# Performance work log

Measured on AMD Instinct MI355X. Metric: run time of the kernel, lower is better.

The kernel has to match this reference:

```python
import jax, jax.numpy as jnp
import numpy as np

N = 4096
D = 128
NUM_INSTANCES = 8  # samples per class in the balanced batch


def setup_inputs() -> dict:
    key = jax.random.key(0)
    x = jax.random.normal(key, (N, D), dtype=jnp.float32)
    # L2-normalize embeddings (keeps sim in [-1,1] so exp(40*sim) is finite)
    inputs = x / jnp.linalg.norm(x, axis=1, keepdims=True)
    # balanced batch: NUM_INSTANCES consecutive samples per class
    targets = (jnp.arange(N) // NUM_INSTANCES).astype(jnp.int64)
    return {"inputs": inputs, "targets": targets, "num_instances": NUM_INSTANCES}


def reference(inputs, targets, num_instances):
    n = inputs.shape[0]
    k = num_instances - 1          # positives per row (excluding self)
    sim = inputs @ inputs.T        # [n, n]

    eye = jnp.eye(n, dtype=bool)
    pos_mask = (targets[:, None] == targets[None, :]) & ~eye
    # category per entry: 0 = positive, 1 = negative, 2 = diagonal
    cat = jnp.where(pos_mask, 0, jnp.where(eye, 2, 1))
    order = jnp.argsort(cat, axis=1, stable=True)  # row-major masked_select order
    sorted_sim = jnp.take_along_axis(sim, order, axis=1)

    pos = jnp.sort(sorted_sim[:, :k], axis=1)          # [n, k]
    neg = jnpp_sort = jnp.sort(sorted_sim[:, k:n - 1], axis=1)  # [n, n-1-k]

    # GaussDistribution used .data[0] -> detached scalars (no grad through stats)
    pos_mean = jax.lax.stop_gradient(jnp.mean(pos, axis=1))
    pos_std = jax.lax.stop_gradient(jnp.sqrt(jnp.mean((pos - pos_mean[:, None]) ** 2, axis=1)))
    neg_mean = jax.lax.stop_gradient(jnp.mean(neg, axis=1))
    neg_std = jax.lax.stop_gradient(jnp.sqrt(jnp.mean((neg - neg_mean[:, None]) ** 2, axis=1)))

    inter = (neg_std * pos_mean + pos_std * neg_mean) / (pos_std + neg_std)
    inter = 0.8 * inter + 0.1                           # [n]

    pos_loss = 0.2 * jnp.mean(jnp.log1p(jnp.exp(-10.0 * (pos - inter[:, None]))), axis=1)

    # keep only negatives above (min positive - 0.05); masked mean per row
    keep = neg > (pos[:, :1] - 0.05)                    # [n, n-1-k] bool
    neg_vals = jnp.log1p(jnp.exp(40.0 * (neg - inter[:, None])))
    cnt = jnp.sum(keep, axis=1)
    neg_loss = 0.05 * jnp.sum(jnp.where(keep, neg_vals, 0.0), axis=1) / jnp.maximum(cnt, 1)

    return jnp.sum(pos_loss + neg_loss) / n
```

## Files before the change

kernel.cpp:

```cpp
#include <hip/hip_runtime.h>
#include <math.h>

namespace {

constexpr int N     = 4096;
constexpr int D     = 128;
constexpr int M     = 8;
constexpr int ROWS  = 16;
constexpr int NT    = 1024;
constexpr int NWAVE = NT / 64;
constexpr int TR    = 256;
constexpr int TBYTES = TR * D * 2;
constexpr int NTILE = N / TR;

using short8 = __attribute__((ext_vector_type(8))) short;
using f32x4  = __attribute__((ext_vector_type(4))) float;

__device__ __forceinline__ float bf2f(unsigned short u) {
    unsigned v = (unsigned)u << 16;
    return __builtin_bit_cast(float, v);
}
__device__ __forceinline__ unsigned short f2bf(float f) {
    unsigned u = __builtin_bit_cast(unsigned, f);
    u += 0x7FFFu + ((u >> 16) & 1u);
    return (unsigned short)(u >> 16);
}
__device__ __forceinline__ float sp_fast(float z) {
    return fmaxf(z, 0.f) + __logf(1.f + __expf(-fabsf(z)));
}

__device__ __forceinline__ void gl_lds16(const void* g, void* l) {
    __builtin_amdgcn_global_load_lds(
        (const __attribute__((address_space(1))) unsigned int*)g,
        (__attribute__((address_space(3))) unsigned int*)l,
        16, 0, 0);
}

__global__ void cvt_kernel(const float* __restrict__ X,
                           unsigned short* __restrict__ Xb,
                           float* __restrict__ out)
{
    const int i = blockIdx.x * blockDim.x + threadIdx.x;
    if (i == 0) out[0] = 0.f;
    const float4 v = reinterpret_cast<const float4*>(X)[i];
    ushort4 r;
    r.x = f2bf(v.x); r.y = f2bf(v.y); r.z = f2bf(v.z); r.w = f2bf(v.w);
    reinterpret_cast<ushort4*>(Xb)[i] = r;
}

__global__ __launch_bounds__(NT, 4)
void mdl_kernel(const unsigned short* __restrict__ Xb, float* __restrict__ out)
{
    extern __shared__ char smem[];
    unsigned short* Bt = reinterpret_cast<unsigned short*>(smem);
    float* posLds = reinterpret_cast<float*>(smem + 2 * TBYTES);
    float* red    = posLds + ROWS * M;
    float* stat   = red + NWAVE * ROWS * 2;

    const int t    = threadIdx.x;
    const int lane = t & 63;
    const int w    = t >> 6;
    const int lr   = lane & 15;
    const int lg   = lane >> 4;
    const int bid  = blockIdx.x;
    const int R0   = bid * ROWS;

    const char* XbB = reinterpret_cast<const char*>(Xb);

    short8 afr0, afr1, afr2, afr3;
    {
        const unsigned short* qrow = Xb + (size_t)(R0 + lr) * D + lg * 8;
        afr0 = *reinterpret_cast<const short8*>(qrow);
        afr1 = *reinterpret_cast<const short8*>(qrow + 32);
        afr2 = *reinterpret_cast<const short8*>(qrow + 64);
        afr3 = *reinterpret_cast<const short8*>(qrow + 96);
    }

    auto STAGE = [&](int tile, int buf) {
        const char* src = XbB + (size_t)tile * TBYTES;
        char* dstb = reinterpret_cast<char*>(Bt) + buf * TBYTES + w * 4096;
#pragma unroll
        for (int r = 0; r < 4; ++r) {
            const int o  = w * 4096 + r * 1024 + lane * 16;
            const int so = o ^ (((o >> 8) & 7) << 4);
            gl_lds16(src + so, dstb + r * 1024);
        }
    };

    float sum4[4] = {0.f, 0.f, 0.f, 0.f};
    float sq4[4]  = {0.f, 0.f, 0.f, 0.f};
    unsigned pk0[NTILE], pk1[NTILE];

    STAGE(0, 0);
    __syncthreads();

#pragma unroll
    for (int k = 0; k < NTILE; ++k) {
        if (k + 1 < NTILE) STAGE(k + 1, (k + 1) & 1);

        const char* bufb  = reinterpret_cast<const char*>(Bt) + (k & 1) * TBYTES;
        const int rowoff  = (w * 16 + lr) * 256;
        const int csw     = (lr & 7) << 4;
        short8 b0 = *reinterpret_cast<const short8*>(bufb + rowoff + ((  0 + lg * 16) ^ csw));
        short8 b1 = *reinterpret_cast<const short8*>(bufb + rowoff + (( 64 + lg * 16) ^ csw));
        short8 b2 = *reinterpret_cast<const short8*>(bufb + rowoff + ((128 + lg * 16) ^ csw));
        short8 b3 = *reinterpret_cast<const short8*>(bufb + rowoff + ((192 + lg * 16) ^ csw));

        f32x4 acc = {0.f, 0.f, 0.f, 0.f};
        acc = __builtin_amdgcn_mfma_f32_16x16x32_bf16(afr0, b0, acc, 0, 0, 0);
        acc = __builtin_amdgcn_mfma_f32_16x16x32_bf16(afr1, b1, acc, 0, 0, 0);
        acc = __builtin_amdgcn_mfma_f32_16x16x32_bf16(afr2, b2, acc, 0, 0, 0);
        acc = __builtin_amdgcn_mfma_f32_16x16x32_bf16(afr3, b3, acc, 0, 0, 0);

        const int chunk = k * 16 + w;
        const bool cls  = (chunk == bid) && ((lr >> 3) == (lg >> 1));
        if (!cls) {
#pragma unroll
            for (int i = 0; i < 4; ++i) {
                const float v = acc[i];
                sum4[i] += v; sq4[i] += v * v;
            }
        } else {
#pragma unroll
            for (int i = 0; i < 4; ++i)
                posLds[(lg * 4 + i) * M + (lr & 7)] = acc[i];
        }
        pk0[k] = (unsigned)f2bf(acc[0]) | ((unsigned)f2bf(acc[1]) << 16);
        pk1[k] = (unsigned)f2bf(acc[2]) | ((unsigned)f2bf(acc[3]) << 16);

        __syncthreads();
    }

#pragma unroll
    for (int i = 0; i < 4; ++i) {
        float s = sum4[i], q = sq4[i];
#pragma unroll
        for (int off = 8; off; off >>= 1) {
            s += __shfl_down(s, off, 16);
            q += __shfl_down(q, off, 16);
        }
        if (lr == 0) {
            red[(w * ROWS + lg * 4 + i) * 2]     = s;
            red[(w * ROWS + lg * 4 + i) * 2 + 1] = q;
        }
    }
    __syncthreads();

    if (t < ROWS) {
        const int r = t;
        float tot = 0.f, totsq = 0.f;
        for (int ww = 0; ww < NWAVE; ++ww) {
            tot   += red[(ww * ROWS + r) * 2];
            totsq += red[(ww * ROWS + r) * 2 + 1];
        }
        float psum = 0.f, psq = 0.f, pmin = 1e30f;
        for (int p = 0; p < M; ++p) {
            if (p == (r & 7)) continue;
            const float s = posLds[r * M + p];
            psum += s; psq += s * s; pmin = fminf(pmin, s);
        }
        const float kinv  = 1.f / (float)(M - 1);
        const float pmean = psum * kinv;
        const float pstd  = sqrtf(fmaxf(psq * kinv - pmean * pmean, 0.f));
        const float ninv  = 1.f / (float)(N - M);
        const float nmean = tot * ninv;
        const float nstd  = sqrtf(fmaxf(totsq * ninv - nmean * nmean, 0.f));
        float inter = (nstd * pmean + pstd * nmean) / (pstd + nstd);
        inter = 0.8f * inter + 0.1f;

        float pl = 0.f;
        for (int p = 0; p < M; ++p) {
            if (p == (r & 7)) continue;
            pl += sp_fast(-10.f * (posLds[r * M + p] - inter));
        }
        pl *= 0.2f * kinv;

        stat[r * 4 + 0] = inter;
        stat[r * 4 + 1] = pmin - 0.05f;
        stat[r * 4 + 2] = pl;
    }
    __syncthreads();

    float itr4[4], thr4[4];
#pragma unroll
    for (int i = 0; i < 4; ++i) {
        itr4[i] = stat[(lg * 4 + i) * 4 + 0];
        thr4[i] = stat[(lg * 4 + i) * 4 + 1];
    }
    float nls[4] = {0.f, 0.f, 0.f, 0.f};
    float cnt[4] = {0.f, 0.f, 0.f, 0.f};

#pragma unroll
    for (int k = 0; k < NTILE; ++k) {
        const int chunk = k * 16 + w;
        const bool cls  = (chunk == bid) && ((lr >> 3) == (lg >> 1));
#pragma unroll
        for (int i = 0; i < 4; ++i) {
            const unsigned pkw = (i < 2) ? pk0[k] : pk1[k];
            const float v = bf2f((unsigned short)(pkw >> ((i & 1) * 16)));
            if (!cls && v > thr4[i]) {
                cnt[i] += 1.f;
                nls[i] += sp_fast(40.f * (v - itr4[i]));
            }
        }
    }

#pragma unroll
    for (int i = 0; i < 4; ++i) {
        float s = nls[i], c = cnt[i];
#pragma unroll
        for (int off = 8; off; off >>= 1) {
            s += __shfl_down(s, off, 16);
            c += __shfl_down(c, off, 16);
        }
        if (lr == 0) {
            red[(w * ROWS + lg * 4 + i) * 2]     = s;
            red[(w * ROWS + lg * 4 + i) * 2 + 1] = c;
        }
    }
    __syncthreads();

    if (t < ROWS) {
        float a = 0.f, b = 0.f;
        for (int ww = 0; ww < NWAVE; ++ww) {
            a += red[(ww * ROWS + t) * 2];
            b += red[(ww * ROWS + t) * 2 + 1];
        }
        stat[t * 4 + 3] = stat[t * 4 + 2] + 0.05f * a / fmaxf(b, 1.f);
    }
    __syncthreads();

    if (t == 0) {
        float acc = 0.f;
        for (int r = 0; r < ROWS; ++r) acc += stat[r * 4 + 3];
        atomicAdd(out, acc * (1.f / (float)N));
    }
}

}

extern "C" void kernel_launch(void* const* d_in, const int* in_sizes, int n_in,
                              void* d_out, int out_size, void* d_ws, size_t ws_size,
                              hipStream_t stream)
{
    const float* X = (const float*)d_in[0];
    float* out = (float*)d_out;
    unsigned short* Xb = (unsigned short*)d_ws;

    cvt_kernel<<<dim3(N * D / 4 / 256), dim3(256), 0, stream>>>(X, Xb, out);

    const size_t shmem = (size_t)2 * TBYTES
                       + (size_t)(ROWS * M) * 4
                       + (size_t)(NWAVE * ROWS * 2) * 4
                       + (size_t)(ROWS * 4) * 4;
    (void)hipFuncSetAttribute(reinterpret_cast<const void*>(mdl_kernel),
                              hipFuncAttributeMaxDynamicSharedMemorySize, (int)shmem);

    mdl_kernel<<<dim3(N / ROWS), dim3(NT), shmem, stream>>>(Xb, out);
}
```

Measured before the change: 93.48 us.

## Load B fragments directly from global with register double-buffering, drop LDS staging

Replaces the LDS-staged, swizzled tile pipeline (global_load_lds plus a barrier per tile) with direct per-wave global loads of B fragments into registers, double-buffered across 16 chunks. This removes the 16 block-wide barriers and the large dynamic LDS allocation, which may allow more resident blocks. It also switches bf16 packing to the HIP intrinsic. The cost is more register pressure and reliance on L2/L1 for reuse of the 1 MB bf16 matrix that all 256 blocks read, with uncoalesced 16-byte row loads.

```diff
diff --git a/kernel.cpp b/kernel.cpp
--- a/kernel.cpp
+++ b/kernel.cpp
@@ -1,4 +1,5 @@
 #include <hip/hip_runtime.h>
+#include <hip/hip_bf16.h>
 #include <math.h>
 
 namespace {
@@ -9,9 +10,7 @@
 constexpr int ROWS  = 16;
 constexpr int NT    = 1024;
 constexpr int NWAVE = NT / 64;
-constexpr int TR    = 256;
-constexpr int TBYTES = TR * D * 2;
-constexpr int NTILE = N / TR;
+constexpr int NCH   = 16;
 
 using short8 = __attribute__((ext_vector_type(8))) short;
 using f32x4  = __attribute__((ext_vector_type(4))) float;
@@ -28,12 +27,11 @@
 __device__ __forceinline__ float sp_fast(float z) {
     return fmaxf(z, 0.f) + __logf(1.f + __expf(-fabsf(z)));
 }
-
-__device__ __forceinline__ void gl_lds16(const void* g, void* l) {
-    __builtin_amdgcn_global_load_lds(
-        (const __attribute__((address_space(1))) unsigned int*)g,
-        (__attribute__((address_space(3))) unsigned int*)l,
-        16, 0, 0);
+__device__ __forceinline__ unsigned pack_bf(float lo, float hi) {
+    __hip_bfloat162 h = __float22bfloat162_rn(make_float2(lo, hi));
+    unsigned u;
+    __builtin_memcpy(&u, &h, 4);
+    return u;
 }
 
 __global__ void cvt_kernel(const float* __restrict__ X,
@@ -51,11 +49,9 @@
 __global__ __launch_bounds__(NT, 4)
 void mdl_kernel(const unsigned short* __restrict__ Xb, float* __restrict__ out)
 {
-    extern __shared__ char smem[];
-    unsigned short* Bt = reinterpret_cast<unsigned short*>(smem);
-    float* posLds = reinterpret_cast<float*>(smem + 2 * TBYTES);
-    float* red    = posLds + ROWS * M;
-    float* stat   = red + NWAVE * ROWS * 2;
+    __shared__ float posLds[ROWS * M];
+    __shared__ float red[NWAVE * ROWS * 2];
+    __shared__ float stat[ROWS * 4];
 
     const int t    = threadIdx.x;
     const int lane = t & 63;
@@ -65,8 +61,6 @@
     const int bid  = blockIdx.x;
     const int R0   = bid * ROWS;
 
-    const char* XbB = reinterpret_cast<const char*>(Xb);
-
     short8 afr0, afr1, afr2, afr3;
     {
         const unsigned short* qrow = Xb + (size_t)(R0 + lr) * D + lg * 8;
@@ -76,43 +70,34 @@
         afr3 = *reinterpret_cast<const short8*>(qrow + 96);
     }
 
-    auto STAGE = [&](int tile, int buf) {
-        const char* src = XbB + (size_t)tile * TBYTES;
-        char* dstb = reinterpret_cast<char*>(Bt) + buf * TBYTES + w * 4096;
-#pragma unroll
-        for (int r = 0; r < 4; ++r) {
-            const int o  = w * 4096 + r * 1024 + lane * 16;
-            const int so = o ^ (((o >> 8) & 7) << 4);
-            gl_lds16(src + so, dstb + r * 1024);
-        }
-    };
+    const unsigned short* bbase = Xb + (size_t)(w * 16 + lr) * D + lg * 8;
 
     float sum4[4] = {0.f, 0.f, 0.f, 0.f};
     float sq4[4]  = {0.f, 0.f, 0.f, 0.f};
-    unsigned pk0[NTILE], pk1[NTILE];
-
-    STAGE(0, 0);
-    __syncthreads();
-
-#pragma unroll
-    for (int k = 0; k < NTILE; ++k) {
-        if (k + 1 < NTILE) STAGE(k + 1, (k + 1) & 1);
-
-        const char* bufb  = reinterpret_cast<const char*>(Bt) + (k & 1) * TBYTES;
-        const int rowoff  = (w * 16 + lr) * 256;
-        const int csw     = (lr & 7) << 4;
-        short8 b0 = *reinterpret_cast<const short8*>(bufb + rowoff + ((  0 + lg * 16) ^ csw));
-        short8 b1 = *reinterpret_cast<const short8*>(bufb + rowoff + (( 64 + lg * 16) ^ csw));
-        short8 b2 = *reinterpret_cast<const short8*>(bufb + rowoff + ((128 + lg * 16) ^ csw));
-        short8 b3 = *reinterpret_cast<const short8*>(bufb + rowoff + ((192 + lg * 16) ^ csw));
+    unsigned pk0[NCH], pk1[NCH];
+
+    short8 bf[2][4];
+#pragma unroll
+    for (int kk = 0; kk < 4; ++kk)
+        bf[0][kk] = *reinterpret_cast<const short8*>(bbase + kk * 32);
+
+#pragma unroll
+    for (int cc = 0; cc < NCH; ++cc) {
+        const int cur = cc & 1, nxt = cur ^ 1;
+        if (cc + 1 < NCH) {
+            const unsigned short* nb = bbase + (size_t)(cc + 1) * 256 * D;
+#pragma unroll
+            for (int kk = 0; kk < 4; ++kk)
+                bf[nxt][kk] = *reinterpret_cast<const short8*>(nb + kk * 32);
+        }
 
         f32x4 acc = {0.f, 0.f, 0.f, 0.f};
-        acc = __builtin_amdgcn_mfma_f32_16x16x32_bf16(afr0, b0, acc, 0, 0, 0);
-        acc = __builtin_amdgcn_mfma_f32_16x16x32_bf16(afr1, b1, acc, 0, 0, 0);
-        acc = __builtin_amdgcn_mfma_f32_16x16x32_bf16(afr2, b2, acc, 0, 0, 0);
-        acc = __builtin_amdgcn_mfma_f32_16x16x32_bf16(afr3, b3, acc, 0, 0, 0);
-
-        const int chunk = k * 16 + w;
+        acc = __builtin_amdgcn_mfma_f32_16x16x32_bf16(afr0, bf[cur][0], acc, 0, 0, 0);
+        acc = __builtin_amdgcn_mfma_f32_16x16x32_bf16(afr1, bf[cur][1], acc, 0, 0, 0);
+        acc = __builtin_amdgcn_mfma_f32_16x16x32_bf16(afr2, bf[cur][2], acc, 0, 0, 0);
+        acc = __builtin_amdgcn_mfma_f32_16x16x32_bf16(afr3, bf[cur][3], acc, 0, 0, 0);
+
+        const int chunk = cc * 16 + w;
         const bool cls  = (chunk == bid) && ((lr >> 3) == (lg >> 1));
         if (!cls) {
 #pragma unroll
@@ -125,10 +110,8 @@
             for (int i = 0; i < 4; ++i)
                 posLds[(lg * 4 + i) * M + (lr & 7)] = acc[i];
         }
-        pk0[k] = (unsigned)f2bf(acc[0]) | ((unsigned)f2bf(acc[1]) << 16);
-        pk1[k] = (unsigned)f2bf(acc[2]) | ((unsigned)f2bf(acc[3]) << 16);
-
-        __syncthreads();
+        pk0[cc] = pack_bf(acc[0], acc[1]);
+        pk1[cc] = pack_bf(acc[2], acc[3]);
     }
 
 #pragma unroll
@@ -191,12 +174,12 @@
     float cnt[4] = {0.f, 0.f, 0.f, 0.f};
 
 #pragma unroll
-    for (int k = 0; k < NTILE; ++k) {
-        const int chunk = k * 16 + w;
+    for (int cc = 0; cc < NCH; ++cc) {
+        const int chunk = cc * 16 + w;
         const bool cls  = (chunk == bid) && ((lr >> 3) == (lg >> 1));
 #pragma unroll
         for (int i = 0; i < 4; ++i) {
-            const unsigned pkw = (i < 2) ? pk0[k] : pk1[k];
+            const unsigned pkw = (i < 2) ? pk0[cc] : pk1[cc];
             const float v = bf2f((unsigned short)(pkw >> ((i & 1) * 16)));
             if (!cls && v > thr4[i]) {
                 cnt[i] += 1.f;
@@ -248,13 +231,5 @@
     unsigned short* Xb = (unsigned short*)d_ws;
 
     cvt_kernel<<<dim3(N * D / 4 / 256), dim3(256), 0, stream>>>(X, Xb, out);
-
-    const size_t shmem = (size_t)2 * TBYTES
-                       + (size_t)(ROWS * M) * 4
-                       + (size_t)(NWAVE * ROWS * 2) * 4
-                       + (size_t)(ROWS * 4) * 4;
-    (void)hipFuncSetAttribute(reinterpret_cast<const void*>(mdl_kernel),
-                              hipFuncAttributeMaxDynamicSharedMemorySize, (int)shmem);
-
-    mdl_kernel<<<dim3(N / ROWS), dim3(NT), shmem, stream>>>(Xb, out);
-}
+    mdl_kernel<<<dim3(N / ROWS), dim3(NT), 0, stream>>>(Xb, out);
+}
```

Result: slower. 105.6 us (+13.0%).
